# Performance work log

Measured on AMD Instinct MI355X. Metric: run time of the kernel, lower is better.

## Reference

```python
import jax, jax.numpy as jnp
import numpy as np
import math

NUM_HEADS = 32
KV_CHANNELS = 128
LAYER_NUMBER = 4
# apply_query_key_layer_scaling=True: norm_factor = sqrt(head_dim) * layer_number,
# then scores are re-multiplied by layer_number in fp32 (numerics trick).
NORM_FACTOR = math.sqrt(KV_CHANNELS) * LAYER_NUMBER
COEFF = float(LAYER_NUMBER)
NEG = -1e9


def setup_inputs() -> dict:
    key = jax.random.key(0)
    k1, k2, k3 = jax.random.split(key, 3)
    b, h, s, d = 2, NUM_HEADS, 2048, KV_CHANNELS
    q = jax.random.normal(k1, (b, h, s, d), dtype=jnp.float32)
    k = jax.random.normal(k2, (b, h, s, d), dtype=jnp.float32)
    v = jax.random.normal(k3, (b, h, s, d), dtype=jnp.float32)
    # additive causal mask: 0 where allowed (j <= i), large negative where masked
    causal = jnp.tril(jnp.ones((s, s), dtype=bool))
    mask = jnp.where(causal, 0.0, NEG).astype(jnp.float32)[None, None, :, :]
    mask = jnp.broadcast_to(mask, (b, 1, s, s))
    return {"query_layer": q, "key_layer": k, "value_layer": v, "attention_mask": mask}


def reference(query_layer, key_layer, value_layer, attention_mask):
    b, h, sq, d = query_layer.shape
    skv = key_layer.shape[2]
    # baddbmm with beta=0, alpha=1/norm_factor  ==  (Q K^T) / norm_factor
    scores = jnp.einsum('bhqd,bhkd->bhqk', query_layer, key_layer) / NORM_FACTOR
    # attention_softmax_in_fp32 + layer scaling coefficient
    scores = scores.astype(jnp.float32) * COEFF
    scores = scores + attention_mask[:, :, :, :skv]
    probs = jax.nn.softmax(scores, axis=-1).astype(value_layer.dtype)
    # dropout p=0.0 -> identity
    context = jnp.einsum('bhqk,bhkd->bhqd', probs, value_layer)
    # transpose to [b, sq, h, d] then merge heads -> [b, sq, h*d]
    context = context.transpose(0, 2, 1, 3).reshape(b, sq, h * d)
    return context
```

## Files before the change

### kernel.cpp

```cpp
#include <hip/hip_runtime.h>
#include <cstdint>
#include <cstddef>

typedef __attribute__((ext_vector_type(8))) __bf16 bf16x8;
typedef __attribute__((ext_vector_type(4))) float f32x4;
typedef __attribute__((ext_vector_type(2))) float f32x2;

#define SEQ 2048
#define DIM 128
#define NHEAD 32
#define NBATCH 2
#define NHEADS_TOTAL (NHEAD * NBATCH)
#define QSC (0.08838834764831845f * 1.4426950408889634f)

#define KV_TILE 32
#define TILES_PER_HEAD (SEQ / KV_TILE)
#define TILE_ELEMS (KV_TILE * DIM)
#define K_WS_BYTES ((size_t)NHEADS_TOTAL * TILES_PER_HEAD * TILE_ELEMS * 2)
#define WS_NEEDED (2 * K_WS_BYTES)

#define PS 40

__device__ __forceinline__ float fexp2(float x) {
#if __has_builtin(__builtin_amdgcn_exp2f)
  return __builtin_amdgcn_exp2f(x);
#else
  return __expf(x * 0.69314718055994531f);
#endif
}

__global__ __launch_bounds__(256) void glm_prepass(const float* __restrict__ Kg,
                                                   const float* __restrict__ Vg,
                                                   __bf16* __restrict__ Kws,
                                                   __bf16* __restrict__ Vws) {
  __shared__ float Vl[32 * 132];
  const int hd = blockIdx.x >> 6;
  const int t  = blockIdx.x & 63;
  const int i  = threadIdx.x;
  const int kv = i >> 3, seg = i & 7;
  const size_t src   = ((size_t)hd * SEQ + (size_t)t * 32 + kv) * DIM + seg * 16;
  const size_t tbase = (size_t)(hd * TILES_PER_HEAD + t) * TILE_ELEMS;

  {
    f32x4 a = *(const f32x4*)(Kg + src);
    f32x4 b = *(const f32x4*)(Kg + src + 4);
    f32x4 c4 = *(const f32x4*)(Kg + src + 8);
    f32x4 d4 = *(const f32x4*)(Kg + src + 12);
    bf16x8 A, B;
#pragma unroll
    for (int j = 0; j < 4; ++j) {
      A[j] = (__bf16)a[j]; A[4 + j] = (__bf16)b[j];
      B[j] = (__bf16)c4[j]; B[4 + j] = (__bf16)d4[j];
    }
    const int cf = kv >> 4, lc = kv & 15, cc = seg >> 1, q0 = (seg & 1) * 2;
    const int chunkA = (cf * 4 + cc) * 64 + q0 * 16 + lc;
    *(bf16x8*)&Kws[tbase + (size_t)chunkA * 8] = A;
    *(bf16x8*)&Kws[tbase + (size_t)(chunkA + 16) * 8] = B;
  }

  {
    f32x4 a = *(const f32x4*)(Vg + src);
    f32x4 b = *(const f32x4*)(Vg + src + 4);
    f32x4 c4 = *(const f32x4*)(Vg + src + 8);
    f32x4 d4 = *(const f32x4*)(Vg + src + 12);
    float* vl = &Vl[kv * 132 + seg * 16];
    *(f32x4*)(vl + 0) = a; *(f32x4*)(vl + 4) = b;
    *(f32x4*)(vl + 8) = c4; *(f32x4*)(vl + 12) = d4;
  }
  __syncthreads();
#pragma unroll
  for (int u = 0; u < 2; ++u) {
    const int ch = i * 2 + u;
    const int nt = ch >> 6, kvg = (ch >> 4) & 3, dd = ch & 15;
    bf16x8 wv;
#pragma unroll
    for (int e = 0; e < 8; ++e) wv[e] = (__bf16)Vl[(kvg * 8 + e) * 132 + nt * 16 + dd];
    *(bf16x8*)&Vws[tbase + (size_t)ch * 8] = wv;
  }
}

__global__ __launch_bounds__(256, 3) void glm_attn_main(const float* __restrict__ Qg,
                                                        const __bf16* __restrict__ Kws,
                                                        const __bf16* __restrict__ Vws,
                                                        float* __restrict__ Out) {
  __shared__ __align__(16) __bf16 Kb[2][TILE_ELEMS];
  __shared__ __align__(16) __bf16 Vb[2][TILE_ELEMS];
  __shared__ __align__(16) __bf16 Pt[4][32 * PS];

  const int tid  = threadIdx.x;
  const int w    = tid >> 6;
  const int lane = tid & 63;
  const int quad = lane >> 4;
  const int lcol = lane & 15;

  const int lin  = (int)blockIdx.x + ((int)blockIdx.y << 4) + ((int)blockIdx.z << 9);
  const int xcd  = lin & 7;
  const int k    = lin >> 3;
  const int head = xcd + ((k >> 4) << 3);
  const int qx   = 15 - (k & 15);
  const int hi   = head & 31, bi = head >> 5;

  const int qb = qx * 128;
  const int hd = bi * NHEAD + hi;

  const float*  Qh   = Qg + (size_t)hd * SEQ * DIM;
  const __bf16* Ksrc = Kws + (size_t)hd * TILES_PER_HEAD * TILE_ELEMS;
  const __bf16* Vsrc = Vws + (size_t)hd * TILES_PER_HEAD * TILE_ELEMS;

  const int T = qx * 4 + 4;
  const int Tfull = qx * 4;

  bf16x8 kst0, kst1, vst0, vst1;

#define PREFETCH_REGS(tt)                                                   \
  {                                                                         \
    const __bf16* ks = Ksrc + (size_t)(tt) * TILE_ELEMS + (size_t)tid * 8;  \
    const __bf16* vs = Vsrc + (size_t)(tt) * TILE_ELEMS + (size_t)tid * 8;  \
    kst0 = *(const bf16x8*)ks;    kst1 = *(const bf16x8*)(ks + 2048);       \
    vst0 = *(const bf16x8*)vs;    vst1 = *(const bf16x8*)(vs + 2048);       \
  }

#define WRITE_LDS(b)                                                        \
  {                                                                         \
    *(bf16x8*)&Kb[b][tid * 8]        = kst0;                                \
    *(bf16x8*)&Kb[b][tid * 8 + 2048] = kst1;                                \
    *(bf16x8*)&Vb[b][tid * 8]        = vst0;                                \
    *(bf16x8*)&Vb[b][tid * 8 + 2048] = vst1;                                \
  }

  PREFETCH_REGS(0);

  bf16x8 qf[2][4];
#pragma unroll
  for (int m = 0; m < 2; ++m) {
    const float* qp = Qh + (size_t)(qb + w * 32 + m * 16 + lcol) * DIM + quad * 8;
#pragma unroll
    for (int c = 0; c < 4; ++c) {
      f32x4 a = *(const f32x4*)(qp + c * 32);
      f32x4 b = *(const f32x4*)(qp + c * 32 + 4);
      bf16x8 t;
#pragma unroll
      for (int j = 0; j < 4; ++j) {
        t[j] = (__bf16)(a[j] * QSC);
        t[4 + j] = (__bf16)(b[j] * QSC);
      }
      qf[m][c] = t;
    }
  }

  f32x4 o[2][8];
#pragma unroll
  for (int m = 0; m < 2; ++m)
#pragma unroll
    for (int n = 0; n < 8; ++n) o[m][n] = f32x4{0.f, 0.f, 0.f, 0.f};
  float lsum[2][4];
#pragma unroll
  for (int m = 0; m < 2; ++m)
#pragma unroll
    for (int r = 0; r < 4; ++r) lsum[m][r] = 0.0f;

  WRITE_LDS(0);
  PREFETCH_REGS(1);

  for (int t = 0; t < T; ++t) {
    const int cur = t & 1;
    __syncthreads();

    const __bf16* Kc = Kb[cur];
    const __bf16* Vc = Vb[cur];

    f32x4 s[2][2];
    s[0][0] = s[0][1] = s[1][0] = s[1][1] = f32x4{0.f, 0.f, 0.f, 0.f};
#pragma unroll
    for (int c = 0; c < 4; ++c) {
      bf16x8 k0 = *(const bf16x8*)&Kc[c * 512 + lane * 8];
      bf16x8 k1 = *(const bf16x8*)&Kc[(4 + c) * 512 + lane * 8];
      s[0][0] = __builtin_amdgcn_mfma_f32_16x16x32_bf16(qf[0][c], k0, s[0][0], 0, 0, 0);
      s[1][0] = __builtin_amdgcn_mfma_f32_16x16x32_bf16(qf[1][c], k0, s[1][0], 0, 0, 0);
      s[0][1] = __builtin_amdgcn_mfma_f32_16x16x32_bf16(qf[0][c], k1, s[0][1], 0, 0, 0);
      s[1][1] = __builtin_amdgcn_mfma_f32_16x16x32_bf16(qf[1][c], k1, s[1][1], 0, 0, 0);
    }

    if (t + 1 < T) {
      if (cur) WRITE_LDS(0) else WRITE_LDS(1)
      if (t + 2 < T) PREFETCH_REGS(t + 2);
    }

    __bf16* pw = Pt[w];
    if (t < Tfull) {
#pragma unroll
      for (int m = 0; m < 2; ++m)
#pragma unroll
        for (int cf = 0; cf < 2; ++cf)
#pragma unroll
          for (int r = 0; r < 4; ++r) {
            const float p = fexp2(fminf(s[m][cf][r], 30.0f));
            lsum[m][r] += p;
            pw[(m * 16 + quad * 4 + r) * PS + cf * 16 + lcol] = (__bf16)p;
          }
    } else {
      const int kvb = t * 32;
#pragma unroll
      for (int m = 0; m < 2; ++m) {
        const int rowb = qb + w * 32 + m * 16 + quad * 4;
#pragma unroll
        for (int cf = 0; cf < 2; ++cf) {
          const int col = kvb + cf * 16 + lcol;
#pragma unroll
          for (int r = 0; r < 4; ++r) {
            const float p = (col <= rowb + r) ? fexp2(fminf(s[m][cf][r], 30.0f)) : 0.0f;
            lsum[m][r] += p;
            pw[(m * 16 + quad * 4 + r) * PS + cf * 16 + lcol] = (__bf16)p;
          }
        }
      }
    }

    bf16x8 pf0 = *(const bf16x8*)&pw[lcol * PS + quad * 8];
    bf16x8 pf1 = *(const bf16x8*)&pw[(16 + lcol) * PS + quad * 8];
#pragma unroll
    for (int nt = 0; nt < 8; ++nt) {
      bf16x8 vf = *(const bf16x8*)&Vc[nt * 512 + lane * 8];
      o[0][nt] = __builtin_amdgcn_mfma_f32_16x16x32_bf16(pf0, vf, o[0][nt], 0, 0, 0);
      o[1][nt] = __builtin_amdgcn_mfma_f32_16x16x32_bf16(pf1, vf, o[1][nt], 0, 0, 0);
    }
  }

#pragma unroll
  for (int m = 0; m < 2; ++m)
#pragma unroll
    for (int r = 0; r < 4; ++r) {
      float v = lsum[m][r];
      v += __shfl_xor(v, 1); v += __shfl_xor(v, 2);
      v += __shfl_xor(v, 4); v += __shfl_xor(v, 8);
      lsum[m][r] = 1.0f / v;
    }
#pragma unroll
  for (int m = 0; m < 2; ++m) {
    const int row0 = qb + w * 32 + m * 16 + quad * 4;
#pragma unroll
    for (int r = 0; r < 4; ++r) {
      const float inv = lsum[m][r];
      float* op = Out + ((size_t)bi * SEQ + row0 + r) * (NHEAD * DIM) + hi * DIM + lcol;
#pragma unroll
      for (int nt = 0; nt < 8; ++nt) op[nt * 16] = o[m][nt][r] * inv;
    }
  }
}

__global__ __launch_bounds__(256, 2) void glm_attn_fused(
    const float* __restrict__ Qg, const float* __restrict__ Kg,
    const float* __restrict__ Vg, float* __restrict__ Out) {
  __shared__ __align__(16) __bf16 Kb[32 * DIM];
  __shared__ __align__(16) __bf16 Vb[32 * DIM];
  __shared__ __align__(16) __bf16 Pt[4][32 * PS];

  const int tid  = threadIdx.x;
  const int w    = tid >> 6;
  const int lane = tid & 63;
  const int quad = lane >> 4;
  const int lcol = lane & 15;

  const int qx = (int)gridDim.x - 1 - (int)blockIdx.x;
  const int qb = qx * 128;
  const int hi = blockIdx.y, bi = blockIdx.z;
  const int hd = bi * NHEAD + hi;

  const float* Qh = Qg + (size_t)hd * SEQ * DIM;
  const float* Kh = Kg + (size_t)hd * SEQ * DIM;
  const float* Vh = Vg + (size_t)hd * SEQ * DIM;

  const float* kbase = Kh + (size_t)lcol * DIM + w * 32 + quad * 8;
  const int vnt = tid >> 5, vkvg = (tid >> 3) & 3, vdd = (tid & 7) * 2;
  const float* vbase = Vh + (size_t)(vkvg * 8) * DIM + vnt * 16 + vdd;

  f32x4 kr0, kr1, kr2, kr3;
  f32x2 vr0, vr1, vr2, vr3, vr4, vr5, vr6, vr7;

#define PREFETCH(tt)                                                  \
  {                                                                   \
    const float* ka = kbase + (size_t)(tt) * (32 * DIM);              \
    kr0 = *(const f32x4*)(ka);                                        \
    kr1 = *(const f32x4*)(ka + 4);                                    \
    kr2 = *(const f32x4*)(ka + 16 * DIM);                             \
    kr3 = *(const f32x4*)(ka + 16 * DIM + 4);                         \
    const float* va = vbase + (size_t)(tt) * (32 * DIM);              \
    vr0 = *(const f32x2*)(va + 0 * DIM);                              \
    vr1 = *(const f32x2*)(va + 1 * DIM);                              \
    vr2 = *(const f32x2*)(va + 2 * DIM);                              \
    vr3 = *(const f32x2*)(va + 3 * DIM);                              \
    vr4 = *(const f32x2*)(va + 4 * DIM);                              \
    vr5 = *(const f32x2*)(va + 5 * DIM);                              \
    vr6 = *(const f32x2*)(va + 6 * DIM);                              \
    vr7 = *(const f32x2*)(va + 7 * DIM);                              \
  }

  PREFETCH(0);

  bf16x8 qf[2][4];
#pragma unroll
  for (int m = 0; m < 2; ++m) {
    const float* qp = Qh + (size_t)(qb + w * 32 + m * 16 + lcol) * DIM + quad * 8;
#pragma unroll
    for (int c = 0; c < 4; ++c) {
      f32x4 a = *(const f32x4*)(qp + c * 32);
      f32x4 b = *(const f32x4*)(qp + c * 32 + 4);
      bf16x8 tq;
#pragma unroll
      for (int j = 0; j < 4; ++j) {
        tq[j] = (__bf16)(a[j] * QSC);
        tq[4 + j] = (__bf16)(b[j] * QSC);
      }
      qf[m][c] = tq;
    }
  }

  f32x4 o[2][8];
#pragma unroll
  for (int m = 0; m < 2; ++m)
#pragma unroll
    for (int n = 0; n < 8; ++n) o[m][n] = f32x4{0.f, 0.f, 0.f, 0.f};
  float lsum[2][4];
#pragma unroll
  for (int m = 0; m < 2; ++m)
#pragma unroll
    for (int r = 0; r < 4; ++r) lsum[m][r] = 0.0f;

  const int T = qx * 4 + 4;
  const int Tfull = qx * 4;

  for (int t = 0; t < T; ++t) {
    __syncthreads();
    {
      bf16x8 sA, sB;
#pragma unroll
      for (int j = 0; j < 4; ++j) {
        sA[j] = (__bf16)kr0[j]; sA[4 + j] = (__bf16)kr1[j];
        sB[j] = (__bf16)kr2[j]; sB[4 + j] = (__bf16)kr3[j];
      }
      *(bf16x8*)&Kb[tid * 8]        = sA;
      *(bf16x8*)&Kb[tid * 8 + 2048] = sB;
      bf16x8 v0, v1;
      v0[0] = (__bf16)vr0[0]; v1[0] = (__bf16)vr0[1];
      v0[1] = (__bf16)vr1[0]; v1[1] = (__bf16)vr1[1];
      v0[2] = (__bf16)vr2[0]; v1[2] = (__bf16)vr2[1];
      v0[3] = (__bf16)vr3[0]; v1[3] = (__bf16)vr3[1];
      v0[4] = (__bf16)vr4[0]; v1[4] = (__bf16)vr4[1];
      v0[5] = (__bf16)vr5[0]; v1[5] = (__bf16)vr5[1];
      v0[6] = (__bf16)vr6[0]; v1[6] = (__bf16)vr6[1];
      v0[7] = (__bf16)vr7[0]; v1[7] = (__bf16)vr7[1];
      *(bf16x8*)&Vb[tid * 16]     = v0;
      *(bf16x8*)&Vb[tid * 16 + 8] = v1;
    }
    __syncthreads();
    if (t + 1 < T) PREFETCH(t + 1);

    f32x4 s[2][2];
    s[0][0] = s[0][1] = s[1][0] = s[1][1] = f32x4{0.f, 0.f, 0.f, 0.f};
#pragma unroll
    for (int c = 0; c < 4; ++c) {
      bf16x8 k0 = *(const bf16x8*)&Kb[c * 512 + lane * 8];
      bf16x8 k1 = *(const bf16x8*)&Kb[(4 + c) * 512 + lane * 8];
      s[0][0] = __builtin_amdgcn_mfma_f32_16x16x32_bf16(qf[0][c], k0, s[0][0], 0, 0, 0);
      s[1][0] = __builtin_amdgcn_mfma_f32_16x16x32_bf16(qf[1][c], k0, s[1][0], 0, 0, 0);
      s[0][1] = __builtin_amdgcn_mfma_f32_16x16x32_bf16(qf[0][c], k1, s[0][1], 0, 0, 0);
      s[1][1] = __builtin_amdgcn_mfma_f32_16x16x32_bf16(qf[1][c], k1, s[1][1], 0, 0, 0);
    }

    __bf16* pw = Pt[w];
    if (t < Tfull) {
#pragma unroll
      for (int m = 0; m < 2; ++m)
#pragma unroll
        for (int cf = 0; cf < 2; ++cf)
#pragma unroll
          for (int r = 0; r < 4; ++r) {
            const float p = fexp2(fminf(s[m][cf][r], 30.0f));
            lsum[m][r] += p;
            pw[(m * 16 + quad * 4 + r) * PS + cf * 16 + lcol] = (__bf16)p;
          }
    } else {
      const int kvb = t * 32;
#pragma unroll
      for (int m = 0; m < 2; ++m) {
        const int rowb = qb + w * 32 + m * 16 + quad * 4;
#pragma unroll
        for (int cf = 0; cf < 2; ++cf) {
          const int col = kvb + cf * 16 + lcol;
#pragma unroll
          for (int r = 0; r < 4; ++r) {
            const float p = (col <= rowb + r) ? fexp2(fminf(s[m][cf][r], 30.0f)) : 0.0f;
            lsum[m][r] += p;
            pw[(m * 16 + quad * 4 + r) * PS + cf * 16 + lcol] = (__bf16)p;
          }
        }
      }
    }

    bf16x8 pf0 = *(const bf16x8*)&pw[lcol * PS + quad * 8];
    bf16x8 pf1 = *(const bf16x8*)&pw[(16 + lcol) * PS + quad * 8];
#pragma unroll
    for (int nt = 0; nt < 8; ++nt) {
      bf16x8 vf = *(const bf16x8*)&Vb[nt * 512 + lane * 8];
      o[0][nt] = __builtin_amdgcn_mfma_f32_16x16x32_bf16(pf0, vf, o[0][nt], 0, 0, 0);
      o[1][nt] = __builtin_amdgcn_mfma_f32_16x16x32_bf16(pf1, vf, o[1][nt], 0, 0, 0);
    }
  }

#pragma unroll
  for (int m = 0; m < 2; ++m)
#pragma unroll
    for (int r = 0; r < 4; ++r) {
      float v = lsum[m][r];
      v += __shfl_xor(v, 1); v += __shfl_xor(v, 2);
      v += __shfl_xor(v, 4); v += __shfl_xor(v, 8);
      lsum[m][r] = 1.0f / v;
    }
#pragma unroll
  for (int m = 0; m < 2; ++m) {
    const int row0 = qb + w * 32 + m * 16 + quad * 4;
#pragma unroll
    for (int r = 0; r < 4; ++r) {
      const float inv = lsum[m][r];
      float* op = Out + ((size_t)bi * SEQ + row0 + r) * (NHEAD * DIM) + hi * DIM + lcol;
#pragma unroll
      for (int nt = 0; nt < 8; ++nt) op[nt * 16] = o[m][nt][r] * inv;
    }
  }
}

extern "C" void kernel_launch(void* const* d_in, const int* in_sizes, int n_in,
                              void* d_out, int out_size, void* d_ws, size_t ws_size,
                              hipStream_t stream) {
  const float* Q = (const float*)d_in[0];
  const float* K = (const float*)d_in[1];
  const float* V = (const float*)d_in[2];
  float* Out = (float*)d_out;

  if (ws_size >= WS_NEEDED) {
    __bf16* Kws = (__bf16*)d_ws;
    __bf16* Vws = (__bf16*)((char*)d_ws + K_WS_BYTES);
    glm_prepass<<<dim3(NHEADS_TOTAL * TILES_PER_HEAD), 256, 0, stream>>>(K, V, Kws, Vws);
    glm_attn_main<<<dim3(SEQ / 128, NHEAD, NBATCH), 256, 0, stream>>>(Q, Kws, Vws, Out);
  } else {
    glm_attn_fused<<<dim3(SEQ / 128, NHEAD, NBATCH), 256, 0, stream>>>(Q, K, V, Out);
  }
}
```

Measured before the change: 363.5 us.

## Drop K prepass, convert fp32 K to bf16 inside main kernel; add MFMA priority

The prepass now converts only V to the bf16 tiled layout. The main kernel loads K directly as fp32 from global memory, converts it in registers and writes it to LDS in the MFMA-friendly layout. This removes one global write and read of the K workspace, at the cost of doubling K load bytes inside the main loop and extra conversion work, which hurts more for later query blocks that reread K. It also wraps the MFMA sections in s_setprio raises.

Measured after the change: 430.1 us. 1.18x slower.

```diff
diff --git a/kernel.cpp b/kernel.cpp
--- a/kernel.cpp
+++ b/kernel.cpp
@@ -16,8 +16,8 @@
 #define KV_TILE 32
 #define TILES_PER_HEAD (SEQ / KV_TILE)
 #define TILE_ELEMS (KV_TILE * DIM)
-#define K_WS_BYTES ((size_t)NHEADS_TOTAL * TILES_PER_HEAD * TILE_ELEMS * 2)
-#define WS_NEEDED (2 * K_WS_BYTES)
+#define V_WS_BYTES ((size_t)NHEADS_TOTAL * TILES_PER_HEAD * TILE_ELEMS * 2)
+#define WS_NEEDED V_WS_BYTES
 
 #define PS 40
 
@@ -29,10 +29,17 @@
 #endif
 }
 
-__global__ __launch_bounds__(256) void glm_prepass(const float* __restrict__ Kg,
-                                                   const float* __restrict__ Vg,
-                                                   __bf16* __restrict__ Kws,
-                                                   __bf16* __restrict__ Vws) {
+__device__ __forceinline__ bf16x8 cvt2(const f32x4 a, const f32x4 b) {
+  bf16x8 r;
+  r[0] = (__bf16)a[0]; r[1] = (__bf16)a[1];
+  r[2] = (__bf16)a[2]; r[3] = (__bf16)a[3];
+  r[4] = (__bf16)b[0]; r[5] = (__bf16)b[1];
+  r[6] = (__bf16)b[2]; r[7] = (__bf16)b[3];
+  return r;
+}
+
+__global__ __launch_bounds__(256) void glm_prepass_v(const float* __restrict__ Vg,
+                                                     __bf16* __restrict__ Vws) {
   __shared__ float Vl[32 * 132];
   const int hd = blockIdx.x >> 6;
   const int t  = blockIdx.x & 63;
@@ -40,23 +47,6 @@
   const int kv = i >> 3, seg = i & 7;
   const size_t src   = ((size_t)hd * SEQ + (size_t)t * 32 + kv) * DIM + seg * 16;
   const size_t tbase = (size_t)(hd * TILES_PER_HEAD + t) * TILE_ELEMS;
-
-  {
-    f32x4 a = *(const f32x4*)(Kg + src);
-    f32x4 b = *(const f32x4*)(Kg + src + 4);
-    f32x4 c4 = *(const f32x4*)(Kg + src + 8);
-    f32x4 d4 = *(const f32x4*)(Kg + src + 12);
-    bf16x8 A, B;
-#pragma unroll
-    for (int j = 0; j < 4; ++j) {
-      A[j] = (__bf16)a[j]; A[4 + j] = (__bf16)b[j];
-      B[j] = (__bf16)c4[j]; B[4 + j] = (__bf16)d4[j];
-    }
-    const int cf = kv >> 4, lc = kv & 15, cc = seg >> 1, q0 = (seg & 1) * 2;
-    const int chunkA = (cf * 4 + cc) * 64 + q0 * 16 + lc;
-    *(bf16x8*)&Kws[tbase + (size_t)chunkA * 8] = A;
-    *(bf16x8*)&Kws[tbase + (size_t)(chunkA + 16) * 8] = B;
-  }
 
   {
     f32x4 a = *(const f32x4*)(Vg + src);
@@ -80,7 +70,7 @@
 }
 
 __global__ __launch_bounds__(256, 3) void glm_attn_main(const float* __restrict__ Qg,
-                                                        const __bf16* __restrict__ Kws,
+                                                        const float* __restrict__ Kg,
                                                         const __bf16* __restrict__ Vws,
                                                         float* __restrict__ Out) {
   __shared__ __align__(16) __bf16 Kb[2][TILE_ELEMS];
@@ -104,26 +94,31 @@
   const int hd = bi * NHEAD + hi;
 
   const float*  Qh   = Qg + (size_t)hd * SEQ * DIM;
-  const __bf16* Ksrc = Kws + (size_t)hd * TILES_PER_HEAD * TILE_ELEMS;
+  const float*  Kh   = Kg + (size_t)hd * SEQ * DIM;
   const __bf16* Vsrc = Vws + (size_t)hd * TILES_PER_HEAD * TILE_ELEMS;
 
   const int T = qx * 4 + 4;
   const int Tfull = qx * 4;
 
-  bf16x8 kst0, kst1, vst0, vst1;
+  const float* Kt0 = Kh + (size_t)lcol * DIM + w * 32 + quad * 8;
+  f32x4 kr0, kr1, kr2, kr3;
+  bf16x8 vst0, vst1;
 
 #define PREFETCH_REGS(tt)                                                   \
   {                                                                         \
-    const __bf16* ks = Ksrc + (size_t)(tt) * TILE_ELEMS + (size_t)tid * 8;  \
+    const float* kp = Kt0 + (size_t)(tt) * (32 * DIM);                      \
+    kr0 = *(const f32x4*)(kp);                                              \
+    kr1 = *(const f32x4*)(kp + 4);                                          \
+    kr2 = *(const f32x4*)(kp + 16 * DIM);                                   \
+    kr3 = *(const f32x4*)(kp + 16 * DIM + 4);                               \
     const __bf16* vs = Vsrc + (size_t)(tt) * TILE_ELEMS + (size_t)tid * 8;  \
-    kst0 = *(const bf16x8*)ks;    kst1 = *(const bf16x8*)(ks + 2048);       \
     vst0 = *(const bf16x8*)vs;    vst1 = *(const bf16x8*)(vs + 2048);       \
   }
 
 #define WRITE_LDS(b)                                                        \
   {                                                                         \
-    *(bf16x8*)&Kb[b][tid * 8]        = kst0;                                \
-    *(bf16x8*)&Kb[b][tid * 8 + 2048] = kst1;                                \
+    *(bf16x8*)&Kb[b][tid * 8]        = cvt2(kr0, kr1);                      \
+    *(bf16x8*)&Kb[b][tid * 8 + 2048] = cvt2(kr2, kr3);                      \
     *(bf16x8*)&Vb[b][tid * 8]        = vst0;                                \
     *(bf16x8*)&Vb[b][tid * 8 + 2048] = vst1;                                \
   }
@@ -171,6 +166,7 @@
 
     f32x4 s[2][2];
     s[0][0] = s[0][1] = s[1][0] = s[1][1] = f32x4{0.f, 0.f, 0.f, 0.f};
+    __builtin_amdgcn_s_setprio(1);
 #pragma unroll
     for (int c = 0; c < 4; ++c) {
       bf16x8 k0 = *(const bf16x8*)&Kc[c * 512 + lane * 8];
@@ -180,6 +176,7 @@
       s[0][1] = __builtin_amdgcn_mfma_f32_16x16x32_bf16(qf[0][c], k1, s[0][1], 0, 0, 0);
       s[1][1] = __builtin_amdgcn_mfma_f32_16x16x32_bf16(qf[1][c], k1, s[1][1], 0, 0, 0);
     }
+    __builtin_amdgcn_s_setprio(0);
 
     if (t + 1 < T) {
       if (cur) WRITE_LDS(0) else WRITE_LDS(1)
@@ -218,12 +215,14 @@
 
     bf16x8 pf0 = *(const bf16x8*)&pw[lcol * PS + quad * 8];
     bf16x8 pf1 = *(const bf16x8*)&pw[(16 + lcol) * PS + quad * 8];
+    __builtin_amdgcn_s_setprio(1);
 #pragma unroll
     for (int nt = 0; nt < 8; ++nt) {
       bf16x8 vf = *(const bf16x8*)&Vc[nt * 512 + lane * 8];
       o[0][nt] = __builtin_amdgcn_mfma_f32_16x16x32_bf16(pf0, vf, o[0][nt], 0, 0, 0);
       o[1][nt] = __builtin_amdgcn_mfma_f32_16x16x32_bf16(pf1, vf, o[1][nt], 0, 0, 0);
     }
+    __builtin_amdgcn_s_setprio(0);
   }
 
 #pragma unroll
@@ -277,7 +276,7 @@
   f32x4 kr0, kr1, kr2, kr3;
   f32x2 vr0, vr1, vr2, vr3, vr4, vr5, vr6, vr7;
 
-#define PREFETCH(tt)                                                  \
+#define PREFETCH_F(tt)                                                \
   {                                                                   \
     const float* ka = kbase + (size_t)(tt) * (32 * DIM);              \
     kr0 = *(const f32x4*)(ka);                                        \
@@ -295,7 +294,7 @@
     vr7 = *(const f32x2*)(va + 7 * DIM);                              \
   }
 
-  PREFETCH(0);
+  PREFETCH_F(0);
 
   bf16x8 qf[2][4];
 #pragma unroll
@@ -353,7 +352,7 @@
       *(bf16x8*)&Vb[tid * 16 + 8] = v1;
     }
     __syncthreads();
-    if (t + 1 < T) PREFETCH(t + 1);
+    if (t + 1 < T) PREFETCH_F(t + 1);
 
     f32x4 s[2][2];
     s[0][0] = s[0][1] = s[1][0] = s[1][1] = f32x4{0.f, 0.f, 0.f, 0.f};
@@ -438,10 +437,9 @@
   float* Out = (float*)d_out;
 
   if (ws_size >= WS_NEEDED) {
-    __bf16* Kws = (__bf16*)d_ws;
-    __bf16* Vws = (__bf16*)((char*)d_ws + K_WS_BYTES);
-    glm_prepass<<<dim3(NHEADS_TOTAL * TILES_PER_HEAD), 256, 0, stream>>>(K, V, Kws, Vws);
-    glm_attn_main<<<dim3(SEQ / 128, NHEAD, NBATCH), 256, 0, stream>>>(Q, Kws, Vws, Out);
+    __bf16* Vws = (__bf16*)d_ws;
+    glm_prepass_v<<<dim3(NHEADS_TOTAL * TILES_PER_HEAD), 256, 0, stream>>>(V, Vws);
+    glm_attn_main<<<dim3(SEQ / 128, NHEAD, NBATCH), 256, 0, stream>>>(Q, K, Vws, Out);
   } else {
     glm_attn_fused<<<dim3(SEQ / 128, NHEAD, NBATCH), 256, 0, stream>>>(Q, K, V, Out);
   }
```
